# Kernel tuning notes

Measured on AMD Instinct MI355X. Metric: run time of the kernel, lower is better.

## Reference

```python
import jax, jax.numpy as jnp
import numpy as np

E = 23   # unique experts
K = 3    # active experts per token

def setup_inputs() -> dict:
    key = jax.random.key(0)
    ks = jax.random.split(key, 11)
    d, h, B, N = 1024, 768, 16, 196
    s = 0.02  # init scale so sigmoid gate is non-saturated
    return {
        "x":      jax.random.normal(ks[0], (B, N, d), jnp.float32),
        "gate_w": jax.random.normal(ks[1], (d, E), jnp.float32) * s,
        "gate_b": jnp.zeros((E,), jnp.float32),
        "w1":     jax.random.normal(ks[2], (E, d, h), jnp.float32) * s,
        "b1":     jnp.zeros((E, h), jnp.float32),
        "w2":     jax.random.normal(ks[3], (E, h, d), jnp.float32) * s,
        "b2":     jnp.zeros((E, d), jnp.float32),
        "ws1":    jax.random.normal(ks[4], (d, h), jnp.float32) * s,
        "bs1":    jnp.zeros((h,), jnp.float32),
        "ws2":    jax.random.normal(ks[5], (h, d), jnp.float32) * s,
        "bs2":    jnp.zeros((d,), jnp.float32),
    }

def reference(x, gate_w, gate_b, w1, b1, w2, b2, ws1, bs1, ws2, bs2):
    o_shape = x.shape
    xt = x.reshape(-1, o_shape[-1])            # [T, d]
    T = xt.shape[0]

    # gating: sigmoid gate, top-3 (the 'bias' buffer in the source is zeros)
    gw = jax.nn.sigmoid(xt @ gate_w + gate_b)  # [T, E]
    top_vals, top_idx = jax.lax.top_k(gw, K)   # [T, K]
    tw = top_vals / top_vals.sum(-1, keepdims=True)

    # dense combine weights: tw scattered to [T, E] (0 for unselected experts)
    w_dense = jnp.zeros_like(gw).at[jnp.arange(T)[:, None], top_idx].add(tw)

    # expert MLPs (dense-masked equivalent of the grouped dispatch)
    hh = jax.nn.gelu(jnp.einsum('td,edh->teh', xt, w1) + b1, approximate=False)
    eo = jnp.einsum('teh,ehd->ted', hh, w2) + b2          # [T, E, d]

    # shared expert
    shared = jax.nn.gelu(xt @ ws1 + bs1, approximate=False) @ ws2 + bs2

    out = shared + jnp.einsum('ted,te->td', eo, w_dense)  # [T, d]

    # aux load-balancing loss
    gwn = gw / gw.sum(-1, keepdims=True)
    P = gwn.mean(0)                                       # [E]
    counts = jnp.zeros((E,), gw.dtype).at[top_idx.reshape(-1)].add(1.0)
    Fv = E * counts / (K * T)
    aux = (P * Fv).sum()

    return out.reshape(o_shape), aux
```

## Files before the change

### kernel.cpp

```cpp
#include <hip/hip_runtime.h>
#include <hip/hip_bf16.h>

#define T_TOK 3136
#define DDIM  1024
#define HDIM  768
#define NEXP  23
#define TOPK  3
#define MTILE 128
#define NTILE 128
#define KTILE 32
#define MAXTILES 128
#define MAX_SLOTS 16384
#define GATE_BLOCKS 1568
#define NBLK_T 13

typedef __attribute__((ext_vector_type(8))) short  short8;
typedef __attribute__((ext_vector_type(4))) short  short4v;
typedef __attribute__((ext_vector_type(2))) short  short2v;
typedef __attribute__((ext_vector_type(4))) float  floatx4;

__device__ __forceinline__ short f2b(float f) {
    union { float f; unsigned u; } v; v.f = f;
    unsigned r = v.u + 0x7FFFu + ((v.u >> 16) & 1u);
    return (short)(r >> 16);
}
__device__ __forceinline__ float b2f(short s) {
    union { unsigned u; float f; } v; v.u = ((unsigned)(unsigned short)s) << 16; return v.f;
}
__device__ __forceinline__ float gelu_exact(float v) {
    return 0.5f * v * (1.0f + erff(v * 0.70710678118654752f));
}
__device__ __forceinline__ void gld16(const short* g, short* l) {
    __builtin_amdgcn_global_load_lds(
        (const __attribute__((address_space(1))) void*)g,
        (__attribute__((address_space(3))) void*)l, 16, 0, 0);
}

__global__ __launch_bounds__(256) void gwt_kernel(const float* __restrict__ gw, float* __restrict__ gwT) {
    __shared__ float tile[32][33];
    const int kt = blockIdx.x;
    const int tx = threadIdx.x & 31, ty = threadIdx.x >> 5;
    #pragma unroll
    for (int i = 0; i < 4; i++) {
        int k = ty + i * 8;
        tile[k][tx] = (tx < NEXP) ? gw[(size_t)(kt * 32 + k) * NEXP + tx] : 0.f;
    }
    __syncthreads();
    #pragma unroll
    for (int i = 0; i < 4; i++) {
        int e = ty + i * 8;
        if (e < 24) gwT[(size_t)e * DDIM + kt * 32 + tx] = tile[tx][e];
    }
}

__global__ __launch_bounds__(256) void prep_w_kernel(
    const float* __restrict__ w1, const float* __restrict__ ws1,
    const float* __restrict__ w2, const float* __restrict__ ws2,
    short* __restrict__ w1t, short* __restrict__ ws1t,
    short* __restrict__ w2t, short* __restrict__ ws2t)
{
    const int z = blockIdx.z;
    const float* src; short* dst; int SK, SN;
    if (z < NEXP + 1) {
        src = (z < NEXP) ? w1 + (size_t)z * DDIM * HDIM : ws1;
        dst = (z < NEXP) ? w1t + (size_t)z * DDIM * HDIM : ws1t;
        SK = DDIM; SN = HDIM;
    } else {
        int e = z - (NEXP + 1);
        src = (e < NEXP) ? w2 + (size_t)e * DDIM * HDIM : ws2;
        dst = (e < NEXP) ? w2t + (size_t)e * DDIM * HDIM : ws2t;
        SK = HDIM; SN = DDIM;
    }
    const int nt = blockIdx.x, kt = blockIdx.y;
    if (nt * 32 >= SN || kt * 64 >= SK) return;
    __shared__ float tile[64][33];
    const int tx = threadIdx.x & 31, ty = threadIdx.x >> 5;
    #pragma unroll
    for (int i = 0; i < 8; i++)
        tile[ty + i * 8][tx] = src[(size_t)(kt * 64 + ty + i * 8) * SN + nt * 32 + tx];
    __syncthreads();
    #pragma unroll
    for (int i = 0; i < 4; i++) {
        int n = ty + i * 8;
        short2v sv = { f2b(tile[2 * tx][n]), f2b(tile[2 * tx + 1][n]) };
        *(short2v*)&dst[(size_t)(nt * 32 + n) * SK + kt * 64 + 2 * tx] = sv;
    }
}

__global__ __launch_bounds__(256) void xcvt_kernel(const float* __restrict__ x, short* __restrict__ xb) {
    int i = blockIdx.x * 256 + threadIdx.x;
    float4 v = ((const float4*)x)[i];
    short4v s = { f2b(v.x), f2b(v.y), f2b(v.z), f2b(v.w) };
    ((short4v*)xb)[i] = s;
}

__global__ __launch_bounds__(256) void gate_kernel(
    const float* __restrict__ x, const float* __restrict__ gwT, const float* __restrict__ gb,
    float* __restrict__ gwn, int* __restrict__ top_idx, float* __restrict__ top_w)
{
    const int tid = threadIdx.x;
    const int lane = tid & 63, wave = tid >> 6;
    const int ebase = wave * 6;
    __shared__ float sg[24];

    for (int t = blockIdx.x; t < T_TOK; t += GATE_BLOCKS) {
        const float4* xr4 = (const float4*)(x + (size_t)t * DDIM);
        float4 xv[4];
        #pragma unroll
        for (int j = 0; j < 4; j++) xv[j] = xr4[j * 64 + lane];

        double a0 = 0, a1 = 0, a2 = 0, a3 = 0, a4 = 0, a5 = 0;
        #pragma unroll
        for (int j = 0; j < 4; j++) {
            const float4* gp = (const float4*)gwT + (size_t)ebase * 256 + j * 64 + lane;
            float4 g0 = gp[0 * 256], g1 = gp[1 * 256], g2 = gp[2 * 256];
            float4 g3 = gp[3 * 256], g4 = gp[4 * 256], g5 = gp[5 * 256];
            float4 xj = xv[j];
            a0 += (double)xj.x * g0.x + (double)xj.y * g0.y + (double)xj.z * g0.z + (double)xj.w * g0.w;
            a1 += (double)xj.x * g1.x + (double)xj.y * g1.y + (double)xj.z * g1.z + (double)xj.w * g1.w;
            a2 += (double)xj.x * g2.x + (double)xj.y * g2.y + (double)xj.z * g2.z + (double)xj.w * g2.w;
            a3 += (double)xj.x * g3.x + (double)xj.y * g3.y + (double)xj.z * g3.z + (double)xj.w * g3.w;
            a4 += (double)xj.x * g4.x + (double)xj.y * g4.y + (double)xj.z * g4.z + (double)xj.w * g4.w;
            a5 += (double)xj.x * g5.x + (double)xj.y * g5.y + (double)xj.z * g5.z + (double)xj.w * g5.w;
        }
        #pragma unroll
        for (int off = 32; off > 0; off >>= 1) {
            a0 += __shfl_xor(a0, off);
            a1 += __shfl_xor(a1, off);
            a2 += __shfl_xor(a2, off);
            a3 += __shfl_xor(a3, off);
            a4 += __shfl_xor(a4, off);
            a5 += __shfl_xor(a5, off);
        }

        if (lane == 0) {
            double av[6] = { a0, a1, a2, a3, a4, a5 };
            #pragma unroll
            for (int i = 0; i < 6; i++) {
                int e = ebase + i;
                if (e < NEXP) {
                    float z = (float)av[i] + gb[e];
                    sg[e] = 1.0f / (1.0f + expf(-z));
                }
            }
        }
        __syncthreads();

        if (tid < NEXP) {
            float s = 0.f;
            #pragma unroll
            for (int e = 0; e < NEXP; e++) s += sg[e];
            gwn[(size_t)t * NEXP + tid] = sg[tid] / s;
        }
        if (tid == 0) {
            float v0 = -1.f, v1 = -1.f, v2 = -1.f; int i0 = 0, i1 = 0, i2 = 0;
            for (int e = 0; e < NEXP; e++) {
                float v = sg[e];
                if (v > v0)      { v2 = v1; i2 = i1; v1 = v0; i1 = i0; v0 = v; i0 = e; }
                else if (v > v1) { v2 = v1; i2 = i1; v1 = v; i1 = e; }
                else if (v > v2) { v2 = v; i2 = e; }
            }
            float ts = v0 + v1 + v2;
            top_idx[t * 3 + 0] = i0; top_w[t * 3 + 0] = v0 / ts;
            top_idx[t * 3 + 1] = i1; top_w[t * 3 + 1] = v1 / ts;
            top_idx[t * 3 + 2] = i2; top_w[t * 3 + 2] = v2 / ts;
        }
        __syncthreads();
    }
}

__global__ __launch_bounds__(256) void hist_kernel(
    const int* __restrict__ top_idx, int* __restrict__ block_hist, int* __restrict__ counts)
{
    __shared__ int h[NEXP];
    const int b = blockIdx.x, tid = threadIdx.x;
    if (tid < NEXP) h[tid] = 0;
    __syncthreads();
    int t = b * 256 + tid;
    if (t < T_TOK) {
        atomicAdd(&h[top_idx[t * 3 + 0]], 1);
        atomicAdd(&h[top_idx[t * 3 + 1]], 1);
        atomicAdd(&h[top_idx[t * 3 + 2]], 1);
    }
    __syncthreads();
    if (tid < NEXP) {
        block_hist[b * NEXP + tid] = h[tid];
        atomicAdd(&counts[tid], h[tid]);
    }
}

__global__ __launch_bounds__(256) void offsets_kernel(
    const int* __restrict__ counts, const int* __restrict__ block_hist,
    int* __restrict__ offs, int* __restrict__ ntl, int* __restrict__ block_base,
    int* __restrict__ slot_t, int* __restrict__ tmap_e, int* __restrict__ tmap_b)
{
    __shared__ int soffs[NEXP + 1];
    if (threadIdx.x == 0) {
        int o = 0, ti = 0;
        for (int e = 0; e < NEXP; e++) {
            int nt = (counts[e] + MTILE - 1) / MTILE;
            ntl[e] = nt; offs[e] = o; soffs[e] = o;
            for (int j = 0; j < nt; j++) { tmap_e[ti] = e; tmap_b[ti] = o + j * MTILE; ti++; }
            o += nt * MTILE;
        }
        int nts = (T_TOK + MTILE - 1) / MTILE;
        ntl[NEXP] = nts; offs[NEXP] = o; soffs[NEXP] = o;
        for (int j = 0; j < nts; j++) { tmap_e[ti] = NEXP; tmap_b[ti] = o + j * MTILE; ti++; }
        o += nts * MTILE;
        offs[NEXP + 1] = o;
        ntl[NEXP + 1] = ti;
    }
    __syncthreads();
    if (threadIdx.x < NEXP) {
        int e = threadIdx.x;
        int run = soffs[e];
        for (int b = 0; b < NBLK_T; b++) {
            block_base[b * NEXP + e] = run;
            run += block_hist[b * NEXP + e];
        }
    }
    for (int i = threadIdx.x; i < MAX_SLOTS; i += 256) slot_t[i] = 0;
}

__global__ __launch_bounds__(256) void scatter_kernel(
    const int* __restrict__ top_idx, const int* __restrict__ offs,
    const int* __restrict__ block_base,
    int* __restrict__ slot_t, int* __restrict__ slot_of)
{
    __shared__ int lfill[NEXP];
    const int b = blockIdx.x, tid = threadIdx.x;
    if (tid < NEXP) lfill[tid] = 0;
    __syncthreads();
    int t = b * 256 + tid;
    if (t < T_TOK) {
        #pragma unroll
        for (int k = 0; k < TOPK; k++) {
            int e = top_idx[t * 3 + k];
            int pos = atomicAdd(&lfill[e], 1);
            int s = block_base[b * NEXP + e] + pos;
            slot_t[s] = t;
            slot_of[t * 4 + k] = s;
        }
        int s = offs[NEXP] + t;
        slot_t[s] = t;
        slot_of[t * 4 + 3] = s;
    }
}

__global__ __launch_bounds__(256) void gemm1_kernel(
    const short* __restrict__ xb,
    const short* __restrict__ w1t, const float* __restrict__ b1,
    const short* __restrict__ ws1t, const float* __restrict__ bs1,
    const int* __restrict__ tmap_e, const int* __restrict__ tmap_b,
    const int* __restrict__ ntl,
    const int* __restrict__ slot_t, short* __restrict__ hh)
{
    if ((int)blockIdx.y >= ntl[NEXP + 1]) return;
    const int e = tmap_e[blockIdx.y];
    const int slot_base = tmap_b[blockIdx.y];
    const int n0 = blockIdx.x * NTILE;
    const short* __restrict__ W  = (e < NEXP) ? (w1t + (size_t)e * DDIM * HDIM) : ws1t;
    const float* __restrict__ Bv = (e < NEXP) ? (b1 + (size_t)e * HDIM) : bs1;

    __shared__ __align__(16) short As[MTILE * KTILE];
    __shared__ __align__(16) short Bs[NTILE * KTILE];
    __shared__ int toks[MTILE];

    const int tid = threadIdx.x;
    for (int i = tid; i < MTILE; i += 256) toks[i] = slot_t[slot_base + i];

    const int lane = tid & 63, wave = tid >> 6;
    const int mbase = (wave & 1) * 64, nbase = (wave >> 1) * 64;
    const int lc = lane & 15, q = lane >> 4;

    const int srow = wave * 16 + (lane >> 2);
    const int c8   = (lane & 3) * 8;

    __syncthreads();
    const short* gA0 = xb + (size_t)toks[srow]      * DDIM + c8;
    const short* gA1 = xb + (size_t)toks[64 + srow] * DDIM + c8;
    const short* gB0 = W + (size_t)(n0 + srow)      * DDIM + c8;
    const short* gB1 = W + (size_t)(n0 + 64 + srow) * DDIM + c8;
    short* lA0 = As + wave * 512;
    short* lA1 = As + 2048 + wave * 512;
    short* lB0 = Bs + wave * 512;
    short* lB1 = Bs + 2048 + wave * 512;

    floatx4 acc[4][4];
    #pragma unroll
    for (int m = 0; m < 4; m++)
        #pragma unroll
        for (int n = 0; n < 4; n++) acc[m][n] = (floatx4)0.f;

    for (int k0 = 0; k0 < DDIM; k0 += KTILE) {
        gld16(gA0 + k0, lA0);
        gld16(gA1 + k0, lA1);
        gld16(gB0 + k0, lB0);
        gld16(gB1 + k0, lB1);
        __syncthreads();
        short8 af[4], bf[4];
        #pragma unroll
        for (int m = 0; m < 4; m++) af[m] = *(const short8*)&As[(mbase + m * 16 + lc) * KTILE + q * 8];
        #pragma unroll
        for (int n = 0; n < 4; n++) bf[n] = *(const short8*)&Bs[(nbase + n * 16 + lc) * KTILE + q * 8];
        #pragma unroll
        for (int m = 0; m < 4; m++)
            #pragma unroll
            for (int n = 0; n < 4; n++)
                acc[m][n] = __builtin_amdgcn_mfma_f32_16x16x32_bf16(af[m], bf[n], acc[m][n], 0, 0, 0);
        __syncthreads();
    }

    #pragma unroll
    for (int n = 0; n < 4; n++) {
        const int col = n0 + nbase + n * 16 + lc;
        const float bb = Bv[col];
        #pragma unroll
        for (int m = 0; m < 4; m++) {
            const int rbase = slot_base + mbase + m * 16 + q * 4;
            #pragma unroll
            for (int r = 0; r < 4; r++) {
                float v = acc[m][n][r] + bb;
                hh[(size_t)(rbase + r) * HDIM + col] = f2b(gelu_exact(v));
            }
        }
    }
}

__global__ __launch_bounds__(256) void gemm2_kernel(
    const short* __restrict__ hh,
    const short* __restrict__ w2t, const float* __restrict__ b2,
    const short* __restrict__ ws2t, const float* __restrict__ bs2,
    const int* __restrict__ tmap_e, const int* __restrict__ tmap_b,
    const int* __restrict__ ntl,
    short* __restrict__ eo)
{
    if ((int)blockIdx.y >= ntl[NEXP + 1]) return;
    const int e = tmap_e[blockIdx.y];
    const int slot_base = tmap_b[blockIdx.y];
    const int n0 = blockIdx.x * NTILE;
    const short* __restrict__ W  = (e < NEXP) ? (w2t + (size_t)e * HDIM * DDIM) : ws2t;
    const float* __restrict__ Bv = (e < NEXP) ? (b2 + (size_t)e * DDIM) : bs2;

    __shared__ __align__(16) short As[MTILE * KTILE];
    __shared__ __align__(16) short Bs[NTILE * KTILE];

    const int tid = threadIdx.x;
    const int lane = tid & 63, wave = tid >> 6;
    const int mbase = (wave & 1) * 64, nbase = (wave >> 1) * 64;
    const int lc = lane & 15, q = lane >> 4;

    const int srow = wave * 16 + (lane >> 2);
    const int c8   = (lane & 3) * 8;

    const short* gA0 = hh + (size_t)(slot_base + srow)      * HDIM + c8;
    const short* gA1 = hh + (size_t)(slot_base + 64 + srow) * HDIM + c8;
    const short* gB0 = W + (size_t)(n0 + srow)      * HDIM + c8;
    const short* gB1 = W + (size_t)(n0 + 64 + srow) * HDIM + c8;
    short* lA0 = As + wave * 512;
    short* lA1 = As + 2048 + wave * 512;
    short* lB0 = Bs + wave * 512;
    short* lB1 = Bs + 2048 + wave * 512;

    floatx4 acc[4][4];
    #pragma unroll
    for (int m = 0; m < 4; m++)
        #pragma unroll
        for (int n = 0; n < 4; n++) acc[m][n] = (floatx4)0.f;

    for (int k0 = 0; k0 < HDIM; k0 += KTILE) {
        gld16(gA0 + k0, lA0);
        gld16(gA1 + k0, lA1);
        gld16(gB0 + k0, lB0);
        gld16(gB1 + k0, lB1);
        __syncthreads();
        short8 af[4], bf[4];
        #pragma unroll
        for (int m = 0; m < 4; m++) af[m] = *(const short8*)&As[(mbase + m * 16 + lc) * KTILE + q * 8];
        #pragma unroll
        for (int n = 0; n < 4; n++) bf[n] = *(const short8*)&Bs[(nbase + n * 16 + lc) * KTILE + q * 8];
        #pragma unroll
        for (int m = 0; m < 4; m++)
            #pragma unroll
            for (int n = 0; n < 4; n++)
                acc[m][n] = __builtin_amdgcn_mfma_f32_16x16x32_bf16(af[m], bf[n], acc[m][n], 0, 0, 0);
        __syncthreads();
    }

    #pragma unroll
    for (int n = 0; n < 4; n++) {
        const int col = n0 + nbase + n * 16 + lc;
        const float bb = Bv[col];
        #pragma unroll
        for (int m = 0; m < 4; m++) {
            const int rbase = slot_base + mbase + m * 16 + q * 4;
            #pragma unroll
            for (int r = 0; r < 4; r++)
                eo[(size_t)(rbase + r) * DDIM + col] = f2b(acc[m][n][r] + bb);
        }
    }
}

__global__ __launch_bounds__(256) void combine_kernel(
    const short* __restrict__ eo, const float* __restrict__ top_w,
    const int* __restrict__ slot_of, float* __restrict__ out)
{
    const int t = blockIdx.x;
    const int c = threadIdx.x * 4;
    const int s0 = slot_of[t * 4 + 0], s1 = slot_of[t * 4 + 1];
    const int s2 = slot_of[t * 4 + 2], s3 = slot_of[t * 4 + 3];
    const float w0 = top_w[t * 3 + 0], w1 = top_w[t * 3 + 1], w2 = top_w[t * 3 + 2];
    short4v a = *(const short4v*)(eo + (size_t)s0 * DDIM + c);
    short4v b = *(const short4v*)(eo + (size_t)s1 * DDIM + c);
    short4v d = *(const short4v*)(eo + (size_t)s2 * DDIM + c);
    short4v s = *(const short4v*)(eo + (size_t)s3 * DDIM + c);
    float4 o;
    o.x = b2f(s.x) + w0 * b2f(a.x) + w1 * b2f(b.x) + w2 * b2f(d.x);
    o.y = b2f(s.y) + w0 * b2f(a.y) + w1 * b2f(b.y) + w2 * b2f(d.y);
    o.z = b2f(s.z) + w0 * b2f(a.z) + w1 * b2f(b.z) + w2 * b2f(d.z);
    o.w = b2f(s.w) + w0 * b2f(a.w) + w1 * b2f(b.w) + w2 * b2f(d.w);
    *(float4*)(out + (size_t)t * DDIM + c) = o;
}

__global__ __launch_bounds__(256) void preduce_kernel(const float* __restrict__ gwn, float* __restrict__ Pf) {
    __shared__ float sP[NEXP];
    if (threadIdx.x < NEXP) sP[threadIdx.x] = 0.f;
    __syncthreads();
    int t = blockIdx.x * blockDim.x + threadIdx.x;
    if (t < T_TOK) {
        #pragma unroll
        for (int e = 0; e < NEXP; e++) atomicAdd(&sP[e], gwn[(size_t)t * NEXP + e]);
    }
    __syncthreads();
    if (threadIdx.x < NEXP) atomicAdd(&Pf[threadIdx.x], sP[threadIdx.x]);
}

__global__ void aux_kernel(const float* __restrict__ Pf, const int* __restrict__ counts,
                           float* __restrict__ out_aux) {
    if (threadIdx.x == 0 && blockIdx.x == 0) {
        float aux = 0.f;
        for (int e = 0; e < NEXP; e++) {
            float P = Pf[e] / (float)T_TOK;
            float F = (float)NEXP * (float)counts[e] / (float)(TOPK * T_TOK);
            aux += P * F;
        }
        out_aux[0] = aux;
    }
}

extern "C" void kernel_launch(void* const* d_in, const int* in_sizes, int n_in,
                              void* d_out, int out_size, void* d_ws, size_t ws_size,
                              hipStream_t stream)
{
    const float* x   = (const float*)d_in[0];
    const float* gw  = (const float*)d_in[1];
    const float* gb  = (const float*)d_in[2];
    const float* w1  = (const float*)d_in[3];
    const float* b1  = (const float*)d_in[4];
    const float* w2  = (const float*)d_in[5];
    const float* b2  = (const float*)d_in[6];
    const float* ws1 = (const float*)d_in[7];
    const float* bs1 = (const float*)d_in[8];
    const float* ws2 = (const float*)d_in[9];
    const float* bs2 = (const float*)d_in[10];
    float* out = (float*)d_out;

    char* p = (char*)d_ws;
    auto alloc = [&](size_t bytes) -> char* {
        char* r = p; p += (bytes + 255) & ~(size_t)255; return r;
    };
    float* gwn      = (float*)alloc((size_t)T_TOK * NEXP * 4);
    int*   top_idx  = (int*)  alloc((size_t)T_TOK * 3 * 4);
    float* top_w    = (float*)alloc((size_t)T_TOK * 3 * 4);
    int*   meta     = (int*)  alloc(2 * NEXP * 4);
    int*   counts   = meta;
    float* Pf       = (float*)(meta + NEXP);
    int*   offs     = (int*)  alloc((NEXP + 2) * 4);
    int*   ntl      = (int*)  alloc((NEXP + 2) * 4);
    int*   bhist    = (int*)  alloc((size_t)NBLK_T * NEXP * 4);
    int*   bbase    = (int*)  alloc((size_t)NBLK_T * NEXP * 4);
    int*   slot_t   = (int*)  alloc((size_t)MAX_SLOTS * 4);
    int*   slot_of  = (int*)  alloc((size_t)T_TOK * 4 * 4);
    int*   tmap_e   = (int*)  alloc((size_t)MAXTILES * 4);
    int*   tmap_b   = (int*)  alloc((size_t)MAXTILES * 4);
    float* gwT      = (float*)alloc((size_t)24 * DDIM * 4);
    short* xb       = (short*)alloc((size_t)T_TOK * DDIM * 2);
    short* w1t      = (short*)alloc((size_t)NEXP * DDIM * HDIM * 2);
    short* ws1t     = (short*)alloc((size_t)DDIM * HDIM * 2);
    short* w2t      = (short*)alloc((size_t)NEXP * DDIM * HDIM * 2);
    short* ws2t     = (short*)alloc((size_t)DDIM * HDIM * 2);
    short* hh       = (short*)alloc((size_t)MAX_SLOTS * HDIM * 2);
    short* eo       = (short*)alloc((size_t)MAX_SLOTS * DDIM * 2);

    hipMemsetAsync(meta, 0, 2 * NEXP * 4, stream);

    gwt_kernel<<<DDIM / 32, 256, 0, stream>>>(gw, gwT);
    prep_w_kernel<<<dim3(32, 16, 2 * (NEXP + 1)), 256, 0, stream>>>(
        w1, ws1, w2, ws2, w1t, ws1t, w2t, ws2t);
    xcvt_kernel<<<(T_TOK * DDIM / 4) / 256, 256, 0, stream>>>(x, xb);
    gate_kernel<<<GATE_BLOCKS, 256, 0, stream>>>(x, gwT, gb, gwn, top_idx, top_w);
    hist_kernel<<<NBLK_T, 256, 0, stream>>>(top_idx, bhist, counts);
    offsets_kernel<<<1, 256, 0, stream>>>(counts, bhist, offs, ntl, bbase, slot_t, tmap_e, tmap_b);
    scatter_kernel<<<NBLK_T, 256, 0, stream>>>(top_idx, offs, bbase, slot_t, slot_of);
    gemm1_kernel<<<dim3(HDIM / NTILE, MAXTILES), 256, 0, stream>>>(
        xb, w1t, b1, ws1t, bs1, tmap_e, tmap_b, ntl, slot_t, hh);
    gemm2_kernel<<<dim3(DDIM / NTILE, MAXTILES), 256, 0, stream>>>(
        hh, w2t, b2, ws2t, bs2, tmap_e, tmap_b, ntl, eo);
    combine_kernel<<<T_TOK, 256, 0, stream>>>(eo, top_w, slot_of, out);
    preduce_kernel<<<(T_TOK + 255) / 256, 256, 0, stream>>>(gwn, Pf);
    aux_kernel<<<1, 64, 0, stream>>>(Pf, counts, out + (size_t)T_TOK * DDIM);
}
```

Measured before the change: 420.0 us.

## Fuse weight transpose and bf16 conversion into the expert GEMM loads

Removes the separate prep_w kernel that transposed and converted all fp32 expert and shared weights to bf16. Each GEMM now reads fp32 weights directly with float2 loads, converts them to bf16 in registers, and writes a transposed, XOR-swizzled, padded LDS tile. This drops a full pass over roughly 150 MB of fp32 weights plus the bf16 writeback. In exchange, the GEMMs issue synchronous fp32 global loads with twice the bytes instead of async LDS loads. Each weight tile is also re-read by every token tile of the same expert.

```diff
diff --git a/kernel.cpp b/kernel.cpp
--- a/kernel.cpp
+++ b/kernel.cpp
@@ -9,6 +9,7 @@
 #define MTILE 128
 #define NTILE 128
 #define KTILE 32
+#define LDSB  40
 #define MAXTILES 128
 #define MAX_SLOTS 16384
 #define GATE_BLOCKS 1568
@@ -50,40 +51,6 @@
     for (int i = 0; i < 4; i++) {
         int e = ty + i * 8;
         if (e < 24) gwT[(size_t)e * DDIM + kt * 32 + tx] = tile[tx][e];
-    }
-}
-
-__global__ __launch_bounds__(256) void prep_w_kernel(
-    const float* __restrict__ w1, const float* __restrict__ ws1,
-    const float* __restrict__ w2, const float* __restrict__ ws2,
-    short* __restrict__ w1t, short* __restrict__ ws1t,
-    short* __restrict__ w2t, short* __restrict__ ws2t)
-{
-    const int z = blockIdx.z;
-    const float* src; short* dst; int SK, SN;
-    if (z < NEXP + 1) {
-        src = (z < NEXP) ? w1 + (size_t)z * DDIM * HDIM : ws1;
-        dst = (z < NEXP) ? w1t + (size_t)z * DDIM * HDIM : ws1t;
-        SK = DDIM; SN = HDIM;
-    } else {
-        int e = z - (NEXP + 1);
-        src = (e < NEXP) ? w2 + (size_t)e * DDIM * HDIM : ws2;
-        dst = (e < NEXP) ? w2t + (size_t)e * DDIM * HDIM : ws2t;
-        SK = HDIM; SN = DDIM;
-    }
-    const int nt = blockIdx.x, kt = blockIdx.y;
-    if (nt * 32 >= SN || kt * 64 >= SK) return;
-    __shared__ float tile[64][33];
-    const int tx = threadIdx.x & 31, ty = threadIdx.x >> 5;
-    #pragma unroll
-    for (int i = 0; i < 8; i++)
-        tile[ty + i * 8][tx] = src[(size_t)(kt * 64 + ty + i * 8) * SN + nt * 32 + tx];
-    __syncthreads();
-    #pragma unroll
-    for (int i = 0; i < 4; i++) {
-        int n = ty + i * 8;
-        short2v sv = { f2b(tile[2 * tx][n]), f2b(tile[2 * tx + 1][n]) };
-        *(short2v*)&dst[(size_t)(nt * 32 + n) * SK + kt * 64 + 2 * tx] = sv;
     }
 }
 
@@ -249,8 +216,8 @@
 
 __global__ __launch_bounds__(256) void gemm1_kernel(
     const short* __restrict__ xb,
-    const short* __restrict__ w1t, const float* __restrict__ b1,
-    const short* __restrict__ ws1t, const float* __restrict__ bs1,
+    const float* __restrict__ w1, const float* __restrict__ b1,
+    const float* __restrict__ ws1, const float* __restrict__ bs1,
     const int* __restrict__ tmap_e, const int* __restrict__ tmap_b,
     const int* __restrict__ ntl,
     const int* __restrict__ slot_t, short* __restrict__ hh)
@@ -259,11 +226,11 @@
     const int e = tmap_e[blockIdx.y];
     const int slot_base = tmap_b[blockIdx.y];
     const int n0 = blockIdx.x * NTILE;
-    const short* __restrict__ W  = (e < NEXP) ? (w1t + (size_t)e * DDIM * HDIM) : ws1t;
+    const float* __restrict__ Wf = (e < NEXP) ? (w1 + (size_t)e * DDIM * HDIM) : ws1;
     const float* __restrict__ Bv = (e < NEXP) ? (b1 + (size_t)e * HDIM) : bs1;
 
     __shared__ __align__(16) short As[MTILE * KTILE];
-    __shared__ __align__(16) short Bs[NTILE * KTILE];
+    __shared__ __align__(16) short Bs[NTILE * LDSB];
     __shared__ int toks[MTILE];
 
     const int tid = threadIdx.x;
@@ -272,6 +239,7 @@
     const int lane = tid & 63, wave = tid >> 6;
     const int mbase = (wave & 1) * 64, nbase = (wave >> 1) * 64;
     const int lc = lane & 15, q = lane >> 4;
+    const int xq8 = (q ^ ((lc >> 1) & 3)) << 3;
 
     const int srow = wave * 16 + (lane >> 2);
     const int c8   = (lane & 3) * 8;
@@ -279,12 +247,14 @@
     __syncthreads();
     const short* gA0 = xb + (size_t)toks[srow]      * DDIM + c8;
     const short* gA1 = xb + (size_t)toks[64 + srow] * DDIM + c8;
-    const short* gB0 = W + (size_t)(n0 + srow)      * DDIM + c8;
-    const short* gB1 = W + (size_t)(n0 + 64 + srow) * DDIM + c8;
     short* lA0 = As + wave * 512;
     short* lA1 = As + 2048 + wave * 512;
-    short* lB0 = Bs + wave * 512;
-    short* lB1 = Bs + 2048 + wave * 512;
+
+    const int g = wave, cn = lane;
+    const float* gW = Wf + (size_t)(8 * g) * HDIM + n0 + 2 * cn;
+    const int bws = (g ^ (cn & 3)) << 3;
+    short* bw0 = Bs + (2 * cn)     * LDSB + bws;
+    short* bw1 = Bs + (2 * cn + 1) * LDSB + bws;
 
     floatx4 acc[4][4];
     #pragma unroll
@@ -295,14 +265,21 @@
     for (int k0 = 0; k0 < DDIM; k0 += KTILE) {
         gld16(gA0 + k0, lA0);
         gld16(gA1 + k0, lA1);
-        gld16(gB0 + k0, lB0);
-        gld16(gB1 + k0, lB1);
+        const float* gp = gW + (size_t)k0 * HDIM;
+        float2 f[8];
+        #pragma unroll
+        for (int j = 0; j < 8; j++) f[j] = *(const float2*)(gp + (size_t)j * HDIM);
+        short8 s0, s1;
+        #pragma unroll
+        for (int j = 0; j < 8; j++) { s0[j] = f2b(f[j].x); s1[j] = f2b(f[j].y); }
+        *(short8*)bw0 = s0;
+        *(short8*)bw1 = s1;
         __syncthreads();
         short8 af[4], bf[4];
         #pragma unroll
         for (int m = 0; m < 4; m++) af[m] = *(const short8*)&As[(mbase + m * 16 + lc) * KTILE + q * 8];
         #pragma unroll
-        for (int n = 0; n < 4; n++) bf[n] = *(const short8*)&Bs[(nbase + n * 16 + lc) * KTILE + q * 8];
+        for (int n = 0; n < 4; n++) bf[n] = *(const short8*)&Bs[(nbase + n * 16 + lc) * LDSB + xq8];
         #pragma unroll
         for (int m = 0; m < 4; m++)
             #pragma unroll
@@ -329,8 +306,8 @@
 
 __global__ __launch_bounds__(256) void gemm2_kernel(
     const short* __restrict__ hh,
-    const short* __restrict__ w2t, const float* __restrict__ b2,
-    const short* __restrict__ ws2t, const float* __restrict__ bs2,
+    const float* __restrict__ w2, const float* __restrict__ b2,
+    const float* __restrict__ ws2, const float* __restrict__ bs2,
     const int* __restrict__ tmap_e, const int* __restrict__ tmap_b,
     const int* __restrict__ ntl,
     short* __restrict__ eo)
@@ -339,28 +316,31 @@
     const int e = tmap_e[blockIdx.y];
     const int slot_base = tmap_b[blockIdx.y];
     const int n0 = blockIdx.x * NTILE;
-    const short* __restrict__ W  = (e < NEXP) ? (w2t + (size_t)e * HDIM * DDIM) : ws2t;
+    const float* __restrict__ Wf = (e < NEXP) ? (w2 + (size_t)e * HDIM * DDIM) : ws2;
     const float* __restrict__ Bv = (e < NEXP) ? (b2 + (size_t)e * DDIM) : bs2;
 
     __shared__ __align__(16) short As[MTILE * KTILE];
-    __shared__ __align__(16) short Bs[NTILE * KTILE];
+    __shared__ __align__(16) short Bs[NTILE * LDSB];
 
     const int tid = threadIdx.x;
     const int lane = tid & 63, wave = tid >> 6;
     const int mbase = (wave & 1) * 64, nbase = (wave >> 1) * 64;
     const int lc = lane & 15, q = lane >> 4;
+    const int xq8 = (q ^ ((lc >> 1) & 3)) << 3;
 
     const int srow = wave * 16 + (lane >> 2);
     const int c8   = (lane & 3) * 8;
 
     const short* gA0 = hh + (size_t)(slot_base + srow)      * HDIM + c8;
     const short* gA1 = hh + (size_t)(slot_base + 64 + srow) * HDIM + c8;
-    const short* gB0 = W + (size_t)(n0 + srow)      * HDIM + c8;
-    const short* gB1 = W + (size_t)(n0 + 64 + srow) * HDIM + c8;
     short* lA0 = As + wave * 512;
     short* lA1 = As + 2048 + wave * 512;
-    short* lB0 = Bs + wave * 512;
-    short* lB1 = Bs + 2048 + wave * 512;
+
+    const int g = wave, cn = lane;
+    const float* gW = Wf + (size_t)(8 * g) * DDIM + n0 + 2 * cn;
+    const int bws = (g ^ (cn & 3)) << 3;
+    short* bw0 = Bs + (2 * cn)     * LDSB + bws;
+    short* bw1 = Bs + (2 * cn + 1) * LDSB + bws;
 
     floatx4 acc[4][4];
     #pragma unroll
@@ -371,14 +351,21 @@
     for (int k0 = 0; k0 < HDIM; k0 += KTILE) {
         gld16(gA0 + k0, lA0);
         gld16(gA1 + k0, lA1);
-        gld16(gB0 + k0, lB0);
-        gld16(gB1 + k0, lB1);
+        const float* gp = gW + (size_t)k0 * DDIM;
+        float2 f[8];
+        #pragma unroll
+        for (int j = 0; j < 8; j++) f[j] = *(const float2*)(gp + (size_t)j * DDIM);
+        short8 s0, s1;
+        #pragma unroll
+        for (int j = 0; j < 8; j++) { s0[j] = f2b(f[j].x); s1[j] = f2b(f[j].y); }
+        *(short8*)bw0 = s0;
+        *(short8*)bw1 = s1;
         __syncthreads();
         short8 af[4], bf[4];
         #pragma unroll
         for (int m = 0; m < 4; m++) af[m] = *(const short8*)&As[(mbase + m * 16 + lc) * KTILE + q * 8];
         #pragma unroll
-        for (int n = 0; n < 4; n++) bf[n] = *(const short8*)&Bs[(nbase + n * 16 + lc) * KTILE + q * 8];
+        for (int n = 0; n < 4; n++) bf[n] = *(const short8*)&Bs[(nbase + n * 16 + lc) * LDSB + xq8];
         #pragma unroll
         for (int m = 0; m < 4; m++)
             #pragma unroll
@@ -485,27 +472,21 @@
     int*   tmap_b   = (int*)  alloc((size_t)MAXTILES * 4);
     float* gwT      = (float*)alloc((size_t)24 * DDIM * 4);
     short* xb       = (short*)alloc((size_t)T_TOK * DDIM * 2);
-    short* w1t      = (short*)alloc((size_t)NEXP * DDIM * HDIM * 2);
-    short* ws1t     = (short*)alloc((size_t)DDIM * HDIM * 2);
-    short* w2t      = (short*)alloc((size_t)NEXP * DDIM * HDIM * 2);
-    short* ws2t     = (short*)alloc((size_t)DDIM * HDIM * 2);
     short* hh       = (short*)alloc((size_t)MAX_SLOTS * HDIM * 2);
     short* eo       = (short*)alloc((size_t)MAX_SLOTS * DDIM * 2);
 
     hipMemsetAsync(meta, 0, 2 * NEXP * 4, stream);
 
     gwt_kernel<<<DDIM / 32, 256, 0, stream>>>(gw, gwT);
-    prep_w_kernel<<<dim3(32, 16, 2 * (NEXP + 1)), 256, 0, stream>>>(
-        w1, ws1, w2, ws2, w1t, ws1t, w2t, ws2t);
     xcvt_kernel<<<(T_TOK * DDIM / 4) / 256, 256, 0, stream>>>(x, xb);
     gate_kernel<<<GATE_BLOCKS, 256, 0, stream>>>(x, gwT, gb, gwn, top_idx, top_w);
     hist_kernel<<<NBLK_T, 256, 0, stream>>>(top_idx, bhist, counts);
     offsets_kernel<<<1, 256, 0, stream>>>(counts, bhist, offs, ntl, bbase, slot_t, tmap_e, tmap_b);
     scatter_kernel<<<NBLK_T, 256, 0, stream>>>(top_idx, offs, bbase, slot_t, slot_of);
     gemm1_kernel<<<dim3(HDIM / NTILE, MAXTILES), 256, 0, stream>>>(
-        xb, w1t, b1, ws1t, bs1, tmap_e, tmap_b, ntl, slot_t, hh);
+        xb, w1, b1, ws1, bs1, tmap_e, tmap_b, ntl, slot_t, hh);
     gemm2_kernel<<<dim3(DDIM / NTILE, MAXTILES), 256, 0, stream>>>(
-        hh, w2t, b2, ws2t, bs2, tmap_e, tmap_b, ntl, eo);
+        hh, w2, b2, ws2, bs2, tmap_e, tmap_b, ntl, eo);
     combine_kernel<<<T_TOK, 256, 0, stream>>>(eo, top_w, slot_of, out);
     preduce_kernel<<<(T_TOK + 255) / 256, 256, 0, stream>>>(gwn, Pf);
     aux_kernel<<<1, 64, 0, stream>>>(Pf, counts, out + (size_t)T_TOK * DDIM);
```

Measured after the change: 424.1 us. Within noise of the previous version (+1.0%).
